# Optimization experiments

Measured on AMD Instinct MI355X. Metric: run time of the kernel, lower is better.

The kernel has to match this reference:

```python
import jax, jax.numpy as jnp
import numpy as np

B, S, H, D = 2, 2048, 16, 64
HID = H * D
NEG = -1e9


def _rope(q, cos, sin):
    # q: (B,S,H,D); cos/sin: (S, D//2) -> broadcast (1,S,1,D//2)
    qe, qo = q[..., 0::2], q[..., 1::2]
    c = cos[None, :, None, :]
    s = sin[None, :, None, :]
    oe = qe * c - qo * s
    oo = qe * s + qo * c
    return jnp.stack([oe, oo], axis=-1).reshape(q.shape)  # interleave even/odd pairs


def setup_inputs() -> dict:
    key = jax.random.key(0)
    ks = jax.random.split(key, 9)
    scale = 1.0 / np.sqrt(HID)
    x = jax.random.normal(ks[0], (B, S, HID), jnp.float32)
    Wq = jax.random.normal(ks[1], (HID, HID), jnp.float32) * scale
    Wk = jax.random.normal(ks[2], (HID, HID), jnp.float32) * scale
    Wv = jax.random.normal(ks[3], (HID, HID), jnp.float32) * scale
    Wo = jax.random.normal(ks[4], (HID, HID), jnp.float32) * scale
    bq = jnp.zeros((HID,), jnp.float32)
    bk = jnp.zeros((HID,), jnp.float32)
    bv = jnp.zeros((HID,), jnp.float32)
    bo = jnp.zeros((HID,), jnp.float32)
    # standard RoPE angles: theta_i = 10000^{-2i/D}
    inv_freq = 1.0 / (10000.0 ** (np.arange(0, D, 2, dtype=np.float32) / D))  # (D/2,)
    angles = jnp.arange(S, dtype=jnp.float32)[:, None] * jnp.asarray(inv_freq)[None, :]
    freqs_cos = jnp.cos(angles)
    freqs_sin = jnp.sin(angles)
    causal = jnp.tril(jnp.ones((S, S), bool))
    mask = jnp.where(causal, 0.0, NEG).astype(jnp.float32)[None, None]  # (1,1,S,S)
    return dict(x=x, Wq=Wq, bq=bq, Wk=Wk, bk=bk, Wv=Wv, bv=bv, Wo=Wo, bo=bo,
                mask=mask, freqs_cos=freqs_cos, freqs_sin=freqs_sin)


def reference(x, Wq, bq, Wk, bk, Wv, bv, Wo, bo, mask, freqs_cos, freqs_sin):
    b, s, hid = x.shape
    # weights stored (in, out): y = x @ W + b (equivalent to torch Linear with W^T)
    q = (x @ Wq + bq).reshape(b, s, H, D)
    k = (x @ Wk + bk).reshape(b, s, H, D)
    v = (x @ Wv + bv).reshape(b, s, H, D)
    q = _rope(q, freqs_cos, freqs_sin)
    k = _rope(k, freqs_cos, freqs_sin)
    q = q.transpose(0, 2, 1, 3)  # (B,H,S,D)
    k = k.transpose(0, 2, 1, 3)
    v = v.transpose(0, 2, 1, 3)
    scores = jnp.einsum('bhqd,bhkd->bhqk', q, k) / np.sqrt(D)
    scores = scores + mask
    attn = jax.nn.softmax(scores.astype(jnp.float32), axis=-1)
    out = jnp.einsum('bhqk,bhkd->bhqd', attn, v)
    out = out.transpose(0, 2, 1, 3).reshape(b, s, hid)
    return out @ Wo + bo
```

## Files before the change

### kernel.cpp

```cpp
#include <hip/hip_runtime.h>
#include <hip/hip_bf16.h>

#define BDIM 2
#define SDIM 2048
#define HDIM 16
#define DDIM 64
#define HID  1024
#define MDIM (BDIM * SDIM)

typedef __attribute__((ext_vector_type(8))) short short8;
typedef __attribute__((ext_vector_type(4))) short short4v;
typedef __attribute__((ext_vector_type(4))) float f32x4;
typedef __attribute__((ext_vector_type(2))) unsigned int uint2v;

__device__ __forceinline__ float bf2f(short u) {
    union { unsigned int i; float f; } x;
    x.i = ((unsigned int)(unsigned short)u) << 16;
    return x.f;
}
__device__ __forceinline__ short f2bf(float f) {
    union { float f; unsigned int i; } x; x.f = f;
    unsigned int r = x.i + 0x7fffu + ((x.i >> 16) & 1u);
    return (short)(r >> 16);
}
__device__ __forceinline__ unsigned int cvtpk_bf16(float lo, float hi) {
    unsigned int r;
    asm("v_cvt_pk_bf16_f32 %0, %1, %2" : "=v"(r) : "v"(lo), "v"(hi));
    return r;
}
__device__ __forceinline__ int swz(int row, int c8) {
    return row * 64 + ((c8 ^ (row & 7)) << 3);
}

__global__ __launch_bounds__(256) void cvt_bf16(const float* __restrict__ in,
                                               short* __restrict__ out, int n) {
    int i = (blockIdx.x * 256 + threadIdx.x) * 8;
    if (i >= n) return;
    float4 a = *(const float4*)(in + i);
    float4 b = *(const float4*)(in + i + 4);
    short8 v;
    v[0] = f2bf(a.x); v[1] = f2bf(a.y); v[2] = f2bf(a.z); v[3] = f2bf(a.w);
    v[4] = f2bf(b.x); v[5] = f2bf(b.y); v[6] = f2bf(b.z); v[7] = f2bf(b.w);
    *(short8*)(out + i) = v;
}

__global__ __launch_bounds__(256) void transpose4(
    const float* __restrict__ w0, const float* __restrict__ w1,
    const float* __restrict__ w2, const float* __restrict__ w3,
    short* __restrict__ o0, short* __restrict__ o1,
    short* __restrict__ o2, short* __restrict__ o3)
{
    const float* src; short* dst;
    int z = blockIdx.z;
    if (z == 0)      { src = w0; dst = o0; }
    else if (z == 1) { src = w1; dst = o1; }
    else if (z == 2) { src = w2; dst = o2; }
    else             { src = w3; dst = o3; }
    __shared__ float t[64][65];
    int r0 = blockIdx.y * 64, c0 = blockIdx.x * 64;
    int rd_r = threadIdx.x >> 4, rd_c = (threadIdx.x & 15) * 4;
    #pragma unroll
    for (int it = 0; it < 4; it++) {
        int rr = rd_r + it * 16;
        float4 v = *(const float4*)(src + (size_t)(r0 + rr) * HID + c0 + rd_c);
        t[rr][rd_c + 0] = v.x; t[rr][rd_c + 1] = v.y;
        t[rr][rd_c + 2] = v.z; t[rr][rd_c + 3] = v.w;
    }
    __syncthreads();
    int or_ = threadIdx.x >> 3, oc8 = (threadIdx.x & 7) * 8;
    #pragma unroll
    for (int half = 0; half < 2; half++) {
        int dr = or_ + half * 32;
        short8 v;
        #pragma unroll
        for (int i = 0; i < 8; i++) v[i] = f2bf(t[oc8 + i][dr]);
        *(short8*)(dst + (size_t)(c0 + dr) * HID + r0 + oc8) = v;
    }
}

__global__ __launch_bounds__(512) void gemm_bf16(
    const short* __restrict__ X,
    const short* __restrict__ Wt0,
    const float* __restrict__ b0, const float* __restrict__ b1, const float* __restrict__ b2,
    const float* __restrict__ cosb, const float* __restrict__ sinb,
    short* __restrict__ out0, float* __restrict__ outf,
    int modeBase)
{
    __shared__ __align__(16) short Asm[2][128 * 32];
    __shared__ __align__(16) short Bsm[2][128 * 32];
    int z = blockIdx.z;
    int mode = modeBase + z;
    const short* Wt = Wt0 + (size_t)z * HID * HID;
    const float* bias = (z == 0) ? b0 : (z == 1) ? b1 : b2;
    short* outp = out0 + (size_t)z * MDIM * HID;

    int tid = threadIdx.x;
    int lane = tid & 63, wave = tid >> 6;
    int wr = wave >> 2, wc = wave & 3;
    int m0 = blockIdx.x * 128, n0 = blockIdx.y * 128;
    int sr = tid >> 2, sc = (tid & 3) * 8;
    int lr = lane & 15, lg = lane >> 4;

    const short* ax = X  + (size_t)(m0 + sr) * HID + sc;
    const short* bx = Wt + (size_t)(n0 + sr) * HID + sc;
    int csw = ((tid & 3) ^ ((sr >> 1) & 3)) * 8;
    int wA  = sr * 32 + csw;
    int rdsw = (lg ^ ((lr >> 1) & 3)) * 8;

    f32x4 acc[4][2] = {};
    constexpr int NK = HID / 32;

    short8 a0, b0v;
    a0  = *(const short8*)(ax);
    b0v = *(const short8*)(bx);
    *(short8*)(Asm[0] + wA) = a0;
    *(short8*)(Bsm[0] + wA) = b0v;
    a0  = *(const short8*)(ax + 32);
    b0v = *(const short8*)(bx + 32);

    int cur = 0;
    for (int ki = 0; ki < NK; ki++) {
        __syncthreads();
        if (ki + 1 < NK) {
            *(short8*)(Asm[cur ^ 1] + wA) = a0;
            *(short8*)(Bsm[cur ^ 1] + wA) = b0v;
        }
        if (ki + 2 < NK) {
            int k0 = (ki + 2) * 32;
            a0  = *(const short8*)(ax + k0);
            b0v = *(const short8*)(bx + k0);
        }
        short8 af[4], bfr[2];
        #pragma unroll
        for (int m = 0; m < 4; m++)
            af[m] = *(const short8*)(Asm[cur] + (wr * 64 + m * 16 + lr) * 32 + rdsw);
        #pragma unroll
        for (int n = 0; n < 2; n++)
            bfr[n] = *(const short8*)(Bsm[cur] + (wc * 32 + n * 16 + lr) * 32 + rdsw);
        __builtin_amdgcn_s_setprio(1);
        #pragma unroll
        for (int m = 0; m < 4; m++)
            #pragma unroll
            for (int n = 0; n < 2; n++)
                acc[m][n] = __builtin_amdgcn_mfma_f32_16x16x32_bf16(af[m], bfr[n], acc[m][n], 0, 0, 0);
        __builtin_amdgcn_s_setprio(0);
        cur ^= 1;
    }

    #pragma unroll
    for (int m = 0; m < 4; m++) {
        #pragma unroll
        for (int n = 0; n < 2; n++) {
            int gr0 = m0 + wr * 64 + m * 16 + lg * 4;
            int gc  = n0 + wc * 32 + n * 16 + lr;
            if (mode == 3) {
                #pragma unroll
                for (int j = 0; j < 4; j++)
                    outf[(size_t)(gr0 + j) * HID + gc] = acc[m][n][j] + bias[gc];
            } else if (mode == 2) {
                int bb = gr0 >> 11, s0 = gr0 & (SDIM - 1);
                int h = gc >> 6, dd = gc & 63;
                short4v pk;
                #pragma unroll
                for (int j = 0; j < 4; j++) pk[j] = f2bf(acc[m][n][j] + bias[gc]);
                *(short4v*)(outp + ((size_t)((bb * HDIM + h) * DDIM + dd)) * SDIM + s0) = pk;
            } else {
                #pragma unroll
                for (int j = 0; j < 4; j++) {
                    int gr = gr0 + j;
                    int bb = gr >> 11, s = gr & (SDIM - 1);
                    int h = gc >> 6, dd = gc & 63;
                    float v = acc[m][n][j] + bias[gc];
                    float p  = __shfl_xor(v, 1);
                    float cc = cosb[s * 32 + (dd >> 1)];
                    float ss = sinb[s * 32 + (dd >> 1)];
                    v = (dd & 1) ? (p * ss + v * cc) : (v * cc - p * ss);
                    outp[((size_t)((bb * HDIM + h) * SDIM + s)) * DDIM + dd] = f2bf(v);
                }
            }
        }
    }
}

__global__ __launch_bounds__(512) void attn_fwd(
    const short* __restrict__ Q,
    const short* __restrict__ K,
    const short* __restrict__ Vt,
    short* __restrict__ O)
{
    __shared__ __align__(16) short Ks0[64 * 64], Ks1[64 * 64];
    __shared__ __align__(16) short Vs0[64 * 64], Vs1[64 * 64];
    __shared__ __align__(16) short Ps[8][16 * 64];
    int bx = blockIdx.x;
    int qA = bx, qB = 31 - bx;
    int bh = blockIdx.y;
    int tid = threadIdx.x;
    int lane = tid & 63, wave = tid >> 6;
    int wv = wave & 3, grp = wave >> 2;
    int lr = lane & 15, lg = lane >> 4;
    const short* qbase  = Q  + ((size_t)bh * SDIM) * DDIM;
    const short* kbase  = K  + ((size_t)bh * SDIM) * DDIM;
    const short* vtbase = Vt + ((size_t)bh * DDIM) * SDIM;

    const float SCALE = 0.125f * 1.44269504088896340736f;

    int qt_own = grp ? qA : qB;
    int qrow = qt_own * 64 + wv * 16 + lr;

    short8 qf[2];
    #pragma unroll
    for (int ks = 0; ks < 2; ks++) {
        short8 a = *(const short8*)(qbase + (size_t)qrow * DDIM + ks * 32 + lg * 8);
        short8 ra;
        #pragma unroll
        for (int i = 0; i < 8; i++) ra[i] = f2bf(bf2f(a[i]) * SCALE);
        qf[ks] = ra;
    }

    f32x4 lacc = {0.f, 0.f, 0.f, 0.f};
    f32x4 oacc[4] = {};

    int sr_ = tid >> 3, sc8 = tid & 7;
    int kw = swz(sr_, sc8);
    int fo[8];
    #pragma unroll
    for (int ks = 0; ks < 2; ks++)
        #pragma unroll
        for (int n = 0; n < 4; n++) fo[ks * 4 + n] = swz(n * 16 + lr, ks * 4 + lg);
    int po[2] = { swz(lr, lg), swz(lr, 4 + lg) };
    int pw[4];
    #pragma unroll
    for (int n = 0; n < 4; n++)
        pw[n] = lr * 64 + (((n * 2 + (lg >> 1)) ^ (lr & 7)) << 3) + (lg & 1) * 4;

    int nt = qB + 1;

    short8 kreg, vreg;
    kreg = *(const short8*)(kbase + (size_t)sr_ * DDIM + sc8 * 8);
    vreg = *(const short8*)(vtbase + (size_t)sr_ * SDIM + sc8 * 8);
    *(short8*)(Ks0 + kw) = kreg;
    *(short8*)(Vs0 + kw) = vreg;
    kreg = *(const short8*)(kbase + (size_t)(64 + sr_) * DDIM + sc8 * 8);
    vreg = *(const short8*)(vtbase + (size_t)sr_ * SDIM + 64 + sc8 * 8);
    const short* kpre = kbase + (size_t)(128 + sr_) * DDIM + sc8 * 8;
    const short* vpre = vtbase + (size_t)sr_ * SDIM + 128 + sc8 * 8;

    auto pv = [&](f32x4 (&st)[4], bool diag, int kt, short* VsC) {
        if (diag) {
            #pragma unroll
            for (int n = 0; n < 4; n++)
                #pragma unroll
                for (int j = 0; j < 4; j++) {
                    int k = kt * 64 + n * 16 + lg * 4 + j;
                    if (k > qrow) st[n][j] = -1e30f;
                }
        }
        #pragma unroll
        for (int n = 0; n < 4; n++) {
            #pragma unroll
            for (int j = 0; j < 4; j++) st[n][j] = exp2f(st[n][j]);
            lacc[n] += (st[n][0] + st[n][1]) + (st[n][2] + st[n][3]);
        }
        #pragma unroll
        for (int n = 0; n < 4; n++) {
            uint2v pk;
            pk[0] = cvtpk_bf16(st[n][0], st[n][1]);
            pk[1] = cvtpk_bf16(st[n][2], st[n][3]);
            *(uint2v*)(Ps[wave] + pw[n]) = pk;
        }
        __builtin_amdgcn_s_setprio(1);
        #pragma unroll
        for (int ks = 0; ks < 2; ks++) {
            short8 pf = *(const short8*)(Ps[wave] + po[ks]);
            #pragma unroll
            for (int n = 0; n < 4; n++) {
                short8 vf = *(const short8*)(VsC + fo[ks * 4 + n]);
                oacc[n] = __builtin_amdgcn_mfma_f32_16x16x32_bf16(pf, vf, oacc[n], 0, 0, 0);
            }
        }
        __builtin_amdgcn_s_setprio(0);
    };

    auto tile = [&](int kt, short* KsC, short* VsC, short* KsN, short* VsN) {
        __syncthreads();
        if (kt + 1 < nt) {
            *(short8*)(KsN + kw) = kreg;
            *(short8*)(VsN + kw) = vreg;
        }
        if (kt + 2 < nt) {
            kreg = *(const short8*)(kpre);
            vreg = *(const short8*)(vpre);
        }
        kpre += 64 * DDIM;
        vpre += 64;

        bool act = grp ? (kt <= qA) : true;
        if (act) {
            f32x4 st[4] = {};
            __builtin_amdgcn_s_setprio(1);
            #pragma unroll
            for (int ks = 0; ks < 2; ks++) {
                short8 kf[4];
                #pragma unroll
                for (int n = 0; n < 4; n++) kf[n] = *(const short8*)(KsC + fo[ks * 4 + n]);
                #pragma unroll
                for (int n = 0; n < 4; n++)
                    st[n] = __builtin_amdgcn_mfma_f32_16x16x32_bf16(kf[n], qf[ks], st[n], 0, 0, 0);
            }
            __builtin_amdgcn_s_setprio(0);
            pv(st, kt == qt_own, kt, VsC);
        }
    };

    for (int kt = 0; kt < nt; kt += 2) {
        tile(kt, Ks0, Vs0, Ks1, Vs1);
        if (kt + 1 < nt) tile(kt + 1, Ks1, Vs1, Ks0, Vs0);
    }

    float l = (lacc[0] + lacc[1]) + (lacc[2] + lacc[3]);
    l += __shfl_xor(l, 16);
    l += __shfl_xor(l, 32);
    int b = bh >> 4, h = bh & 15;
    float linv[4];
    #pragma unroll
    for (int j = 0; j < 4; j++)
        linv[j] = 1.f / __int_as_float(__builtin_amdgcn_ds_bpermute((lg * 4 + j) * 4, __float_as_int(l)));
    #pragma unroll
    for (int n = 0; n < 4; n++)
        #pragma unroll
        for (int j = 0; j < 4; j++) {
            int s = qt_own * 64 + wv * 16 + lg * 4 + j;
            int dd = n * 16 + lr;
            O[(((size_t)(b * SDIM + s) * HDIM) + h) * DDIM + dd] = f2bf(oacc[n][j] * linv[j]);
        }
}

extern "C" void kernel_launch(void* const* d_in, const int* in_sizes, int n_in,
                              void* d_out, int out_size, void* d_ws, size_t ws_size,
                              hipStream_t stream) {
    const float* x  = (const float*)d_in[0];
    const float* Wq = (const float*)d_in[1];
    const float* bq = (const float*)d_in[2];
    const float* Wk = (const float*)d_in[3];
    const float* bk = (const float*)d_in[4];
    const float* Wv = (const float*)d_in[5];
    const float* bv = (const float*)d_in[6];
    const float* Wo = (const float*)d_in[7];
    const float* bo = (const float*)d_in[8];
    const float* fc = (const float*)d_in[10];
    const float* fs = (const float*)d_in[11];
    float* out = (float*)d_out;
    short* ws  = (short*)d_ws;

    const size_t MM = (size_t)HID * HID;
    short* xb     = ws;
    short* wt_qkv = ws + 4 * MM;
    short* wot    = ws + 7 * MM;
    short* qt     = ws + 8 * MM;
    short* ktb    = ws + 12 * MM;
    short* vtb    = ws + 16 * MM;
    short* ao     = ws + 20 * MM;

    cvt_bf16<<<dim3((MDIM * HID) / (256 * 8)), 256, 0, stream>>>(x, xb, MDIM * HID);
    transpose4<<<dim3(16, 16, 4), 256, 0, stream>>>(Wq, Wk, Wv, Wo,
                                                    wt_qkv, wt_qkv + MM, wt_qkv + 2 * MM, wot);
    gemm_bf16<<<dim3(MDIM / 128, HID / 128, 3), 512, 0, stream>>>(
        xb, wt_qkv, bq, bk, bv, fc, fs, qt, nullptr, 0);
    attn_fwd<<<dim3(16, BDIM * HDIM), 512, 0, stream>>>(qt, ktb, vtb, ao);
    gemm_bf16<<<dim3(MDIM / 128, HID / 128, 1), 512, 0, stream>>>(
        ao, wot, bo, bo, bo, fc, fs, nullptr, out, 3);
}
```

Measured before the change: 103.2 us.

## Merge prep kernels and stage K/V in 128-key chunks per barrier

The x-to-bf16 conversion and the four weight transposes now run in a single prep launch, selected by block index, which saves one kernel launch. In attention, each pipeline stage now loads two 64-key K/V tiles into a double-buffered 128-key chunk, so there is one __syncthreads per two key tiles instead of one per tile. This costs twice the shared memory for K/V and more prefetch registers, which may reduce occupancy. Blocks with an odd tile count leave half of the last chunk idle.

```diff
diff --git a/kernel.cpp b/kernel.cpp
--- a/kernel.cpp
+++ b/kernel.cpp
@@ -32,32 +32,33 @@
     return row * 64 + ((c8 ^ (row & 7)) << 3);
 }
 
-__global__ __launch_bounds__(256) void cvt_bf16(const float* __restrict__ in,
-                                               short* __restrict__ out, int n) {
-    int i = (blockIdx.x * 256 + threadIdx.x) * 8;
-    if (i >= n) return;
-    float4 a = *(const float4*)(in + i);
-    float4 b = *(const float4*)(in + i + 4);
-    short8 v;
-    v[0] = f2bf(a.x); v[1] = f2bf(a.y); v[2] = f2bf(a.z); v[3] = f2bf(a.w);
-    v[4] = f2bf(b.x); v[5] = f2bf(b.y); v[6] = f2bf(b.z); v[7] = f2bf(b.w);
-    *(short8*)(out + i) = v;
-}
-
-__global__ __launch_bounds__(256) void transpose4(
+__global__ __launch_bounds__(256) void prep(
+    const float* __restrict__ x, short* __restrict__ xb,
     const float* __restrict__ w0, const float* __restrict__ w1,
     const float* __restrict__ w2, const float* __restrict__ w3,
     short* __restrict__ o0, short* __restrict__ o1,
     short* __restrict__ o2, short* __restrict__ o3)
 {
+    int bid = blockIdx.x;
+    if (bid < 2048) {
+        int i = (bid * 256 + threadIdx.x) * 8;
+        float4 a = *(const float4*)(x + i);
+        float4 b = *(const float4*)(x + i + 4);
+        short8 v;
+        v[0] = f2bf(a.x); v[1] = f2bf(a.y); v[2] = f2bf(a.z); v[3] = f2bf(a.w);
+        v[4] = f2bf(b.x); v[5] = f2bf(b.y); v[6] = f2bf(b.z); v[7] = f2bf(b.w);
+        *(short8*)(xb + i) = v;
+        return;
+    }
+    __shared__ float t[64][65];
+    int b = bid - 2048;
+    int z = b >> 8, rem = b & 255;
     const float* src; short* dst;
-    int z = blockIdx.z;
     if (z == 0)      { src = w0; dst = o0; }
     else if (z == 1) { src = w1; dst = o1; }
     else if (z == 2) { src = w2; dst = o2; }
     else             { src = w3; dst = o3; }
-    __shared__ float t[64][65];
-    int r0 = blockIdx.y * 64, c0 = blockIdx.x * 64;
+    int r0 = (rem >> 4) * 64, c0 = (rem & 15) * 64;
     int rd_r = threadIdx.x >> 4, rd_c = (threadIdx.x & 15) * 4;
     #pragma unroll
     for (int it = 0; it < 4; it++) {
@@ -188,8 +189,8 @@
     const short* __restrict__ Vt,
     short* __restrict__ O)
 {
-    __shared__ __align__(16) short Ks0[64 * 64], Ks1[64 * 64];
-    __shared__ __align__(16) short Vs0[64 * 64], Vs1[64 * 64];
+    __shared__ __align__(16) short Ks[2][2][64 * 64];
+    __shared__ __align__(16) short Vs[2][2][64 * 64];
     __shared__ __align__(16) short Ps[8][16 * 64];
     int bx = blockIdx.x;
     int qA = bx, qB = 31 - bx;
@@ -233,25 +234,34 @@
     for (int n = 0; n < 4; n++)
         pw[n] = lr * 64 + (((n * 2 + (lg >> 1)) ^ (lr & 7)) << 3) + (lg & 1) * 4;
 
-    int nt = qB + 1;
-
-    short8 kreg, vreg;
-    kreg = *(const short8*)(kbase + (size_t)sr_ * DDIM + sc8 * 8);
-    vreg = *(const short8*)(vtbase + (size_t)sr_ * SDIM + sc8 * 8);
-    *(short8*)(Ks0 + kw) = kreg;
-    *(short8*)(Vs0 + kw) = vreg;
-    kreg = *(const short8*)(kbase + (size_t)(64 + sr_) * DDIM + sc8 * 8);
-    vreg = *(const short8*)(vtbase + (size_t)sr_ * SDIM + 64 + sc8 * 8);
-    const short* kpre = kbase + (size_t)(128 + sr_) * DDIM + sc8 * 8;
-    const short* vpre = vtbase + (size_t)sr_ * SDIM + 128 + sc8 * 8;
-
-    auto pv = [&](f32x4 (&st)[4], bool diag, int kt, short* VsC) {
+    int nt64 = qB + 1;
+    int npairs = qB / 2 + 1;
+
+    short8 kA, kB, vA, vB;
+    kA = *(const short8*)(kbase + (size_t)sr_ * DDIM + sc8 * 8);
+    kB = *(const short8*)(kbase + (size_t)(64 + sr_) * DDIM + sc8 * 8);
+    vA = *(const short8*)(vtbase + (size_t)sr_ * SDIM + sc8 * 8);
+    vB = *(const short8*)(vtbase + (size_t)sr_ * SDIM + 64 + sc8 * 8);
+    *(short8*)(Ks[0][0] + kw) = kA;
+    *(short8*)(Ks[0][1] + kw) = kB;
+    *(short8*)(Vs[0][0] + kw) = vA;
+    *(short8*)(Vs[0][1] + kw) = vB;
+    if (npairs > 1) {
+        kA = *(const short8*)(kbase + (size_t)(128 + sr_) * DDIM + sc8 * 8);
+        kB = *(const short8*)(kbase + (size_t)(192 + sr_) * DDIM + sc8 * 8);
+        vA = *(const short8*)(vtbase + (size_t)sr_ * SDIM + 128 + sc8 * 8);
+        vB = *(const short8*)(vtbase + (size_t)sr_ * SDIM + 192 + sc8 * 8);
+    }
+    const short* kpre = kbase + (size_t)(256 + sr_) * DDIM + sc8 * 8;
+    const short* vpre = vtbase + (size_t)sr_ * SDIM + 256 + sc8 * 8;
+
+    auto pv = [&](f32x4 (&st)[4], bool diag, int k64, short* VsC) {
         if (diag) {
             #pragma unroll
             for (int n = 0; n < 4; n++)
                 #pragma unroll
                 for (int j = 0; j < 4; j++) {
-                    int k = kt * 64 + n * 16 + lg * 4 + j;
+                    int k = k64 * 64 + n * 16 + lg * 4 + j;
                     if (k > qrow) st[n][j] = -1e30f;
                 }
         }
@@ -281,40 +291,47 @@
         __builtin_amdgcn_s_setprio(0);
     };
 
-    auto tile = [&](int kt, short* KsC, short* VsC, short* KsN, short* VsN) {
+    int cur = 0;
+    for (int kt = 0; kt < npairs; kt++) {
         __syncthreads();
-        if (kt + 1 < nt) {
-            *(short8*)(KsN + kw) = kreg;
-            *(short8*)(VsN + kw) = vreg;
-        }
-        if (kt + 2 < nt) {
-            kreg = *(const short8*)(kpre);
-            vreg = *(const short8*)(vpre);
-        }
-        kpre += 64 * DDIM;
-        vpre += 64;
-
-        bool act = grp ? (kt <= qA) : true;
-        if (act) {
-            f32x4 st[4] = {};
-            __builtin_amdgcn_s_setprio(1);
-            #pragma unroll
-            for (int ks = 0; ks < 2; ks++) {
-                short8 kf[4];
-                #pragma unroll
-                for (int n = 0; n < 4; n++) kf[n] = *(const short8*)(KsC + fo[ks * 4 + n]);
-                #pragma unroll
-                for (int n = 0; n < 4; n++)
-                    st[n] = __builtin_amdgcn_mfma_f32_16x16x32_bf16(kf[n], qf[ks], st[n], 0, 0, 0);
+        if (kt + 1 < npairs) {
+            *(short8*)(Ks[cur ^ 1][0] + kw) = kA;
+            *(short8*)(Ks[cur ^ 1][1] + kw) = kB;
+            *(short8*)(Vs[cur ^ 1][0] + kw) = vA;
+            *(short8*)(Vs[cur ^ 1][1] + kw) = vB;
+        }
+        if (kt + 2 < npairs) {
+            kA = *(const short8*)(kpre);
+            kB = *(const short8*)(kpre + (size_t)64 * DDIM);
+            vA = *(const short8*)(vpre);
+            vB = *(const short8*)(vpre + 64);
+        }
+        kpre += (size_t)128 * DDIM;
+        vpre += 128;
+
+        #pragma unroll
+        for (int h = 0; h < 2; h++) {
+            int k64 = kt * 2 + h;
+            if (k64 >= nt64) continue;
+            bool act = grp ? (k64 <= qA) : true;
+            if (act) {
+                f32x4 st[4] = {};
+                __builtin_amdgcn_s_setprio(1);
+                #pragma unroll
+                for (int ks = 0; ks < 2; ks++) {
+                    short8 kf[4];
+                    #pragma unroll
+                    for (int n = 0; n < 4; n++)
+                        kf[n] = *(const short8*)(Ks[cur][h] + fo[ks * 4 + n]);
+                    #pragma unroll
+                    for (int n = 0; n < 4; n++)
+                        st[n] = __builtin_amdgcn_mfma_f32_16x16x32_bf16(kf[n], qf[ks], st[n], 0, 0, 0);
+                }
+                __builtin_amdgcn_s_setprio(0);
+                pv(st, k64 == qt_own, k64, Vs[cur][h]);
             }
-            __builtin_amdgcn_s_setprio(0);
-            pv(st, kt == qt_own, kt, VsC);
-        }
-    };
-
-    for (int kt = 0; kt < nt; kt += 2) {
-        tile(kt, Ks0, Vs0, Ks1, Vs1);
-        if (kt + 1 < nt) tile(kt + 1, Ks1, Vs1, Ks0, Vs0);
+        }
+        cur ^= 1;
     }
 
     float l = (lacc[0] + lacc[1]) + (lacc[2] + lacc[3]);
@@ -361,9 +378,8 @@
     short* vtb    = ws + 16 * MM;
     short* ao     = ws + 20 * MM;
 
-    cvt_bf16<<<dim3((MDIM * HID) / (256 * 8)), 256, 0, stream>>>(x, xb, MDIM * HID);
-    transpose4<<<dim3(16, 16, 4), 256, 0, stream>>>(Wq, Wk, Wv, Wo,
-                                                    wt_qkv, wt_qkv + MM, wt_qkv + 2 * MM, wot);
+    prep<<<dim3(3072), 256, 0, stream>>>(x, xb, Wq, Wk, Wv, Wo,
+                                         wt_qkv, wt_qkv + MM, wt_qkv + 2 * MM, wot);
     gemm_bf16<<<dim3(MDIM / 128, HID / 128, 3), 512, 0, stream>>>(
         xb, wt_qkv, bq, bk, bv, fc, fs, qt, nullptr, 0);
     attn_fwd<<<dim3(16, BDIM * HDIM), 512, 0, stream>>>(qt, ktb, vtb, ao);
```

After: 102.9 us. No clear change (-0.2%).
